# Kernel optimization log

Measured on AMD Instinct MI355X. Metric: run time of the kernel, lower is better.

Reference implementation:

```python
import jax, jax.numpy as jnp
import numpy as np

N_NODES = 50000
N_EDGES = 800000
N_FEAT = 128
HIDDEN = 128
N_GRAPHS = 256


def gcn_conv(x, W, b, src, dst, n_nodes):
    # PyG GCNConv, add_self_loops=False, edge_weight=1:
    # out_i = sum_{(j->i)} d_j^{-1/2} d_i^{-1/2} (x_j @ W) + b, deg over target idx
    h = x @ W                                    # [N, out]
    deg = jax.ops.segment_sum(jnp.ones((src.shape[0],), h.dtype), dst,
                              num_segments=n_nodes)          # [N]
    dis = jnp.where(deg > 0, jax.lax.rsqrt(jnp.maximum(deg, 1.0)), 0.0)
    norm = dis[src] * dis[dst]                   # [E]
    msg = h[src] * norm[:, None]                 # [E, out] gather + scale
    out = jax.ops.segment_sum(msg, dst, num_segments=n_nodes)  # scatter-add
    return out + b


def setup_inputs() -> dict:
    key = jax.random.key(0)
    ks = jax.random.split(key, 12)
    x = jax.random.normal(ks[0], (N_NODES, N_FEAT), jnp.float32)
    edge_index = jax.random.randint(ks[1], (2, N_EDGES), 0, N_NODES, jnp.int64)
    batch = jnp.sort(jax.random.randint(ks[2], (N_NODES,), 0, N_GRAPHS, jnp.int64))

    def glorot(k, shape):
        lim = float(np.sqrt(6.0 / (shape[0] + shape[1])))
        return jax.random.uniform(k, shape, jnp.float32, -lim, lim)

    W1 = glorot(ks[3], (N_FEAT, HIDDEN)); b1 = jnp.zeros((HIDDEN,), jnp.float32)
    W2 = glorot(ks[4], (HIDDEN, HIDDEN)); b2 = jnp.zeros((HIDDEN,), jnp.float32)
    Wf1 = glorot(ks[5], (HIDDEN, HIDDEN // 2)); bf1 = jnp.zeros((HIDDEN // 2,), jnp.float32)
    Wl = glorot(ks[6], (HIDDEN // 2, 2)); bl = jnp.zeros((2,), jnp.float32)
    return {"x": x, "edge_index": edge_index, "batch": batch,
            "W1": W1, "b1": b1, "W2": W2, "b2": b2,
            "Wf1": Wf1, "bf1": bf1, "Wl": Wl, "bl": bl}


def reference(x, edge_index, batch, W1, b1, W2, b2, Wf1, bf1, Wl, bl):
    src, dst = edge_index[0], edge_index[1]
    h = jax.nn.relu(gcn_conv(x, W1, b1, src, dst, N_NODES))
    h = jax.nn.relu(gcn_conv(h, W2, b2, src, dst, N_NODES))
    h = gcn_conv(h, W2, b2, src, dst, N_NODES)   # conv2 applied a second time (same weights)
    # global_mean_pool over graphs
    sums = jax.ops.segment_sum(h, batch, num_segments=N_GRAPHS)      # [G, H]
    cnts = jax.ops.segment_sum(jnp.ones((h.shape[0],), h.dtype), batch,
                               num_segments=N_GRAPHS)                # [G]
    g = sums / jnp.maximum(cnts, 1.0)[:, None]
    g = jax.nn.relu(g @ Wf1 + bf1)
    logits = g @ Wl + bl
    return jax.nn.softmax(logits, axis=1)
```

## Files before the change

### kernel.cpp

```cpp
#include <hip/hip_runtime.h>
#include <hip/hip_bf16.h>

#define N_NODES 50000
#define N_EDGES 800000
#define NF 128
#define NG 256
#define CAP 64
#define NSEG 256
#define SEGE (N_EDGES / NSEG)
#define NPAD 50048

typedef unsigned short ushort_t;
typedef unsigned char uchar_t;
typedef __attribute__((ext_vector_type(8))) short bf16x8;
typedef __attribute__((ext_vector_type(4))) float f32x4;

__device__ __forceinline__ float b2f(ushort_t u) {
    union { unsigned i; float f; } x; x.i = ((unsigned)u) << 16; return x.f;
}
__device__ __forceinline__ ushort_t f2b(float f) {
    union { float f; unsigned i; } x; x.f = f;
    unsigned r = (x.i + 0x7fffu + ((x.i >> 16) & 1u)) >> 16;
    return (ushort_t)r;
}

__global__ __launch_bounds__(512) void k_seg_count(
        const int* __restrict__ dst, uchar_t* __restrict__ segcnt,
        float* __restrict__ gsum) {
    __shared__ unsigned int cntw[NPAD / 4];
    int tid = threadIdx.x;
    int b = blockIdx.x;
    if (b < 16) {
        ((float4*)gsum)[b * 512 + tid] = make_float4(0.f, 0.f, 0.f, 0.f);
    }
    for (int i = tid; i < NPAD / 4; i += 512) cntw[i] = 0;
    __syncthreads();
    const int* d0 = dst + b * SEGE;
    for (int e = tid; e < SEGE; e += 512) {
        int d = d0[e];
        atomicAdd(&cntw[d >> 2], 1u << ((d & 3) * 8));
    }
    __syncthreads();
    unsigned int* outw = (unsigned int*)(segcnt + (size_t)b * NPAD);
    for (int i = tid; i < NPAD / 4; i += 512) outw[i] = cntw[i];
}

__global__ void k_seg_scan(const uchar_t* __restrict__ segcnt,
                           uchar_t* __restrict__ segbase,
                           int* __restrict__ deg, float* __restrict__ dis) {
    int node = blockIdx.x * 256 + threadIdx.x;
    if (node >= N_NODES) return;
    int run = 0;
#pragma unroll 8
    for (int s = 0; s < NSEG; ++s) {
        size_t idx = (size_t)s * NPAD + node;
        int c = segcnt[idx];
        segbase[idx] = (uchar_t)min(run, 255);
        run += c;
    }
    deg[node] = min(run, CAP);
    dis[node] = (run > 0) ? rsqrtf((float)run) : 0.f;
}

__global__ __launch_bounds__(512) void k_seg_fill(
        const int* __restrict__ src, const int* __restrict__ dst,
        const uchar_t* __restrict__ segbase, ushort_t* __restrict__ csr_pad) {
    __shared__ unsigned int cntw[NPAD / 4];
    int tid = threadIdx.x;
    int b = blockIdx.x;
    for (int i = tid; i < NPAD / 4; i += 512) cntw[i] = 0;
    __syncthreads();
    const int* d0 = dst + b * SEGE;
    const int* s0 = src + b * SEGE;
    const uchar_t* brow = segbase + (size_t)b * NPAD;
    for (int e = tid; e < SEGE; e += 512) {
        int d = d0[e];
        int sh = (d & 3) * 8;
        unsigned old = atomicAdd(&cntw[d >> 2], 1u << sh);
        int pos = (old >> sh) & 0xFF;
        int slot = brow[d] + pos;
        if (slot < CAP) csr_pad[(size_t)d * CAP + slot] = (ushort_t)s0[e];
    }
}

__global__ void k_prep_w2(const float* __restrict__ W1, const float* __restrict__ W2,
                          ushort_t* __restrict__ W1h, ushort_t* __restrict__ W1l,
                          ushort_t* __restrict__ W2h, ushort_t* __restrict__ W2l) {
    int t = blockIdx.x * blockDim.x + threadIdx.x;
    int which = t >> 14;
    int u = t & 16383;
    int k = u >> 7, c = u & 127;
    const float* W = which ? W2 : W1;
    ushort_t* Wh = which ? W2h : W1h;
    ushort_t* Wl = which ? W2l : W1l;
    float w = W[k * 128 + c];
    ushort_t hi = f2b(w);
    ushort_t lo = f2b(w - b2f(hi));
    Wh[c * 128 + k] = hi;
    Wl[c * 128 + k] = lo;
}

template <bool F32A>
__global__ __launch_bounds__(256) void k_gemm_mfma(
        const float* __restrict__ Xf, const ushort_t* __restrict__ Xb,
        const ushort_t* __restrict__ Wt_hi, const ushort_t* __restrict__ Wt_lo,
        const float* __restrict__ dis, ushort_t* __restrict__ Yb, int n) {
    __shared__ ushort_t Wlds[2][16384];
    int t = threadIdx.x;
    {
        const int4* gh = (const int4*)Wt_hi;
        const int4* gl = (const int4*)Wt_lo;
        int4* sh = (int4*)&Wlds[0][0];
        int4* sl = (int4*)&Wlds[1][0];
#pragma unroll
        for (int i = 0; i < 8; ++i) {
            int u = t + i * 256;
            int swz = u ^ ((u >> 4) & 7);
            sh[swz] = gh[u];
            sl[swz] = gl[u];
        }
    }
    __syncthreads();

    int wid = t >> 6;
    int l   = t & 63;
    int la  = l & 15;
    int kb  = l >> 4;
    int r0  = blockIdx.x * 64 + wid * 16;

    bf16x8 a[4];
    {
        int ra = min(r0 + la, n - 1);
        if (F32A) {
            const float* xrow = Xf + (size_t)ra * 128 + kb * 8;
#pragma unroll
            for (int kt = 0; kt < 4; ++kt) {
                float4 v0 = *(const float4*)(xrow + kt * 32);
                float4 v1 = *(const float4*)(xrow + kt * 32 + 4);
                bf16x8 av;
                av[0] = (short)f2b(v0.x); av[1] = (short)f2b(v0.y);
                av[2] = (short)f2b(v0.z); av[3] = (short)f2b(v0.w);
                av[4] = (short)f2b(v1.x); av[5] = (short)f2b(v1.y);
                av[6] = (short)f2b(v1.z); av[7] = (short)f2b(v1.w);
                a[kt] = av;
            }
        } else {
            const ushort_t* xrow = Xb + (size_t)ra * 128 + kb * 8;
#pragma unroll
            for (int kt = 0; kt < 4; ++kt)
                a[kt] = *(const bf16x8*)(xrow + kt * 32);
        }
    }

    f32x4 acc[8];
#pragma unroll
    for (int ct = 0; ct < 8; ++ct) acc[ct] = (f32x4){0.f, 0.f, 0.f, 0.f};

#pragma unroll
    for (int ct = 0; ct < 8; ++ct) {
        int c = ct * 16 + la;
        int ubase = c * 128 + kb * 8;
        int sw = (c & 7) << 3;
#pragma unroll
        for (int kt = 0; kt < 4; ++kt) {
            int u16 = (ubase + kt * 32) ^ sw;
            bf16x8 bh = *(const bf16x8*)&Wlds[0][u16];
            bf16x8 bl = *(const bf16x8*)&Wlds[1][u16];
            acc[ct] = __builtin_amdgcn_mfma_f32_16x16x32_bf16(a[kt], bh, acc[ct], 0, 0, 0);
            acc[ct] = __builtin_amdgcn_mfma_f32_16x16x32_bf16(a[kt], bl, acc[ct], 0, 0, 0);
        }
    }

    float dsc[4];
#pragma unroll
    for (int j = 0; j < 4; ++j)
        dsc[j] = dis[min(r0 + kb * 4 + j, n - 1)];

    __syncthreads();
    ushort_t* tile = ((ushort_t*)Wlds) + wid * 2048;
#pragma unroll
    for (int ct = 0; ct < 8; ++ct) {
        int cc = ct * 16 + la;
#pragma unroll
        for (int j = 0; j < 4; ++j)
            tile[(kb * 4 + j) * 128 + cc] = f2b(acc[ct][j] * dsc[j]);
    }
    __syncthreads();
    {
        const int4* t4 = (const int4*)tile;
        int4* dst4 = (int4*)(Yb + (size_t)r0 * 128);
#pragma unroll
        for (int i = 0; i < 4; ++i) {
            int u = l * 4 + i;
            int row = u >> 4;
            if (r0 + row < n) dst4[u] = t4[u];
        }
    }
}

template <bool RELU>
__global__ __launch_bounds__(256) void k_agg(
        const ushort_t* __restrict__ Hs, const int* __restrict__ deg,
        const ushort_t* __restrict__ csr_pad, const float* __restrict__ dis,
        const float* __restrict__ bias, ushort_t* __restrict__ out, int n) {
    int lane = threadIdx.x & 31;
    int sub  = threadIdx.x >> 5;
    int node = blockIdx.x * 8 + sub;
    if (node >= n) return;
    int dg = deg[node];
    const ushort_t* lst = csr_pad + (size_t)node * CAP;
    int c0 = lane * 4;

    float4 a0 = make_float4(0.f, 0.f, 0.f, 0.f);
    float4 a1 = make_float4(0.f, 0.f, 0.f, 0.f);
    float4 a2 = make_float4(0.f, 0.f, 0.f, 0.f);
    float4 a3 = make_float4(0.f, 0.f, 0.f, 0.f);
    float4 a4 = make_float4(0.f, 0.f, 0.f, 0.f);
    float4 a5 = make_float4(0.f, 0.f, 0.f, 0.f);
    float4 a6 = make_float4(0.f, 0.f, 0.f, 0.f);
    float4 a7 = make_float4(0.f, 0.f, 0.f, 0.f);
    int p = 0;
    for (; p + 7 < dg; p += 8) {
        int j0 = lst[p],     j1 = lst[p + 1], j2 = lst[p + 2], j3 = lst[p + 3];
        int j4 = lst[p + 4], j5 = lst[p + 5], j6 = lst[p + 6], j7 = lst[p + 7];
        ushort4 v0 = *(const ushort4*)&Hs[(size_t)j0 * 128 + c0];
        ushort4 v1 = *(const ushort4*)&Hs[(size_t)j1 * 128 + c0];
        ushort4 v2 = *(const ushort4*)&Hs[(size_t)j2 * 128 + c0];
        ushort4 v3 = *(const ushort4*)&Hs[(size_t)j3 * 128 + c0];
        ushort4 v4 = *(const ushort4*)&Hs[(size_t)j4 * 128 + c0];
        ushort4 v5 = *(const ushort4*)&Hs[(size_t)j5 * 128 + c0];
        ushort4 v6 = *(const ushort4*)&Hs[(size_t)j6 * 128 + c0];
        ushort4 v7 = *(const ushort4*)&Hs[(size_t)j7 * 128 + c0];
        a0.x += b2f(v0.x); a0.y += b2f(v0.y); a0.z += b2f(v0.z); a0.w += b2f(v0.w);
        a1.x += b2f(v1.x); a1.y += b2f(v1.y); a1.z += b2f(v1.z); a1.w += b2f(v1.w);
        a2.x += b2f(v2.x); a2.y += b2f(v2.y); a2.z += b2f(v2.z); a2.w += b2f(v2.w);
        a3.x += b2f(v3.x); a3.y += b2f(v3.y); a3.z += b2f(v3.z); a3.w += b2f(v3.w);
        a4.x += b2f(v4.x); a4.y += b2f(v4.y); a4.z += b2f(v4.z); a4.w += b2f(v4.w);
        a5.x += b2f(v5.x); a5.y += b2f(v5.y); a5.z += b2f(v5.z); a5.w += b2f(v5.w);
        a6.x += b2f(v6.x); a6.y += b2f(v6.y); a6.z += b2f(v6.z); a6.w += b2f(v6.w);
        a7.x += b2f(v7.x); a7.y += b2f(v7.y); a7.z += b2f(v7.z); a7.w += b2f(v7.w);
    }
    for (; p + 3 < dg; p += 4) {
        int j0 = lst[p], j1 = lst[p + 1], j2 = lst[p + 2], j3 = lst[p + 3];
        ushort4 v0 = *(const ushort4*)&Hs[(size_t)j0 * 128 + c0];
        ushort4 v1 = *(const ushort4*)&Hs[(size_t)j1 * 128 + c0];
        ushort4 v2 = *(const ushort4*)&Hs[(size_t)j2 * 128 + c0];
        ushort4 v3 = *(const ushort4*)&Hs[(size_t)j3 * 128 + c0];
        a0.x += b2f(v0.x); a0.y += b2f(v0.y); a0.z += b2f(v0.z); a0.w += b2f(v0.w);
        a1.x += b2f(v1.x); a1.y += b2f(v1.y); a1.z += b2f(v1.z); a1.w += b2f(v1.w);
        a2.x += b2f(v2.x); a2.y += b2f(v2.y); a2.z += b2f(v2.z); a2.w += b2f(v2.w);
        a3.x += b2f(v3.x); a3.y += b2f(v3.y); a3.z += b2f(v3.z); a3.w += b2f(v3.w);
    }
    for (; p < dg; ++p) {
        int j = lst[p];
        ushort4 v = *(const ushort4*)&Hs[(size_t)j * 128 + c0];
        a0.x += b2f(v.x); a0.y += b2f(v.y); a0.z += b2f(v.z); a0.w += b2f(v.w);
    }
    float dsc = dis[node];
    float4 b = *(const float4*)&bias[c0];
    float rx = (((a0.x + a1.x) + (a2.x + a3.x)) + ((a4.x + a5.x) + (a6.x + a7.x))) * dsc + b.x;
    float ry = (((a0.y + a1.y) + (a2.y + a3.y)) + ((a4.y + a5.y) + (a6.y + a7.y))) * dsc + b.y;
    float rz = (((a0.z + a1.z) + (a2.z + a3.z)) + ((a4.z + a5.z) + (a6.z + a7.z))) * dsc + b.z;
    float rw = (((a0.w + a1.w) + (a2.w + a3.w)) + ((a4.w + a5.w) + (a6.w + a7.w))) * dsc + b.w;
    if (RELU) {
        rx = fmaxf(rx, 0.f); ry = fmaxf(ry, 0.f);
        rz = fmaxf(rz, 0.f); rw = fmaxf(rw, 0.f);
    }
    ushort4 o;
    o.x = f2b(rx); o.y = f2b(ry); o.z = f2b(rz); o.w = f2b(rw);
    *(ushort4*)&out[(size_t)node * 128 + c0] = o;
}

#define POOL_CHUNK 128
__global__ __launch_bounds__(128) void k_pool_partial(
        const ushort_t* __restrict__ H, const int* __restrict__ batch,
        float* __restrict__ gsum, int n) {
    int f = threadIdx.x;
    int s = blockIdx.x * POOL_CHUNK;
    int e = min(s + POOL_CHUNK, n);
    if (s >= n) return;
    float acc = 0.f;
    int g = batch[s];
    for (int i = s; i < e; ++i) {
        int bg = batch[i];
        if (bg != g) {
            atomicAdd(&gsum[g * 128 + f], acc);
            acc = 0.f;
            g = bg;
        }
        acc += b2f(H[(size_t)i * 128 + f]);
    }
    atomicAdd(&gsum[g * 128 + f], acc);
}

__global__ void k_head(const float* __restrict__ gsum, const int* __restrict__ batch,
                       const float* __restrict__ Wf1, const float* __restrict__ bf1,
                       const float* __restrict__ Wl, const float* __restrict__ bl,
                       float* __restrict__ out, int n) {
    int g = blockIdx.x;
    int j = threadIdx.x;
    __shared__ float xs[128];
    __shared__ float hs[64];

    int lo = 0, hi = n;
    while (lo < hi) { int m = (lo + hi) >> 1; if (batch[m] < g) lo = m + 1; else hi = m; }
    int s0 = lo;
    hi = n;
    while (lo < hi) { int m = (lo + hi) >> 1; if (batch[m] <= g) lo = m + 1; else hi = m; }
    float inv_cnt = 1.f / fmaxf((float)(lo - s0), 1.f);

    xs[j]      = gsum[g * 128 + j] * inv_cnt;
    xs[j + 64] = gsum[g * 128 + 64 + j] * inv_cnt;
    __syncthreads();
    float acc = bf1[j];
#pragma unroll 4
    for (int k = 0; k < 128; k++) acc += xs[k] * Wf1[k * 64 + j];
    hs[j] = fmaxf(acc, 0.f);
    __syncthreads();
    if (j == 0) {
        float l0 = bl[0], l1 = bl[1];
        for (int k = 0; k < 64; k++) { l0 += hs[k] * Wl[k * 2 + 0]; l1 += hs[k] * Wl[k * 2 + 1]; }
        float m  = fmaxf(l0, l1);
        float e0 = expf(l0 - m), e1 = expf(l1 - m);
        float inv = 1.f / (e0 + e1);
        out[g * 2 + 0] = e0 * inv;
        out[g * 2 + 1] = e1 * inv;
    }
}

extern "C" void kernel_launch(void* const* d_in, const int* in_sizes, int n_in,
                              void* d_out, int out_size, void* d_ws, size_t ws_size,
                              hipStream_t stream) {
    const float* x    = (const float*)d_in[0];
    const int*   eidx = (const int*)d_in[1];
    const int*   batch= (const int*)d_in[2];
    const float* W1   = (const float*)d_in[3];
    const float* b1   = (const float*)d_in[4];
    const float* W2   = (const float*)d_in[5];
    const float* b2   = (const float*)d_in[6];
    const float* Wf1  = (const float*)d_in[7];
    const float* bf1  = (const float*)d_in[8];
    const float* Wl   = (const float*)d_in[9];
    const float* bl   = (const float*)d_in[10];
    float* out = (float*)d_out;

    const int* src = eidx;
    const int* dst = eidx + N_EDGES;

    char* w = (char*)d_ws;
    auto alloc = [&](size_t bytes) -> void* {
        void* p = (void*)w;
        w += (bytes + 255) & ~(size_t)255;
        return p;
    };
    ushort_t* Yb     = (ushort_t*)alloc((size_t)N_NODES * NF * 2);
    ushort_t* Hb     = (ushort_t*)alloc((size_t)N_NODES * NF * 2);
    ushort_t* W1h    = (ushort_t*)alloc((size_t)NF * NF * 2);
    ushort_t* W1l    = (ushort_t*)alloc((size_t)NF * NF * 2);
    ushort_t* W2h    = (ushort_t*)alloc((size_t)NF * NF * 2);
    ushort_t* W2l    = (ushort_t*)alloc((size_t)NF * NF * 2);
    float*    dis    = (float*)alloc((size_t)N_NODES * 4);
    int*      deg    = (int*)  alloc((size_t)N_NODES * 4);
    ushort_t* csr_pad= (ushort_t*)alloc((size_t)N_NODES * CAP * 2);
    uchar_t*  segcnt = (uchar_t*)alloc((size_t)NSEG * NPAD);
    uchar_t*  segbase= (uchar_t*)alloc((size_t)NSEG * NPAD);
    float*    gsum   = (float*)alloc((size_t)NG * NF * 4);

    k_seg_count<<<NSEG, 512, 0, stream>>>(dst, segcnt, gsum);
    k_seg_scan<<<(N_NODES + 255) / 256, 256, 0, stream>>>(segcnt, segbase, deg, dis);
    k_seg_fill<<<NSEG, 512, 0, stream>>>(src, dst, segbase, csr_pad);

    k_prep_w2<<<128, 256, 0, stream>>>(W1, W2, W1h, W1l, W2h, W2l);

    int gb = (N_NODES + 63) / 64;
    int ab = (N_NODES + 7) / 8;
    k_gemm_mfma<true><<<gb, 256, 0, stream>>>(x, nullptr, W1h, W1l, dis, Yb, N_NODES);
    k_agg<true><<<ab, 256, 0, stream>>>(Yb, deg, csr_pad, dis, b1, Hb, N_NODES);
    k_gemm_mfma<false><<<gb, 256, 0, stream>>>(nullptr, Hb, W2h, W2l, dis, Yb, N_NODES);
    k_agg<true><<<ab, 256, 0, stream>>>(Yb, deg, csr_pad, dis, b2, Hb, N_NODES);
    k_gemm_mfma<false><<<gb, 256, 0, stream>>>(nullptr, Hb, W2h, W2l, dis, Yb, N_NODES);
    k_agg<false><<<ab, 256, 0, stream>>>(Yb, deg, csr_pad, dis, b2, Hb, N_NODES);

    k_pool_partial<<<(N_NODES + POOL_CHUNK - 1) / POOL_CHUNK, 128, 0, stream>>>(Hb, batch, gsum, N_NODES);
    k_head<<<NG, 64, 0, stream>>>(gsum, batch, Wf1, bf1, Wl, bl, out, N_NODES);
}
```

Before: 234.6 us.

## Fuse aggregation with next-layer GEMM and fold weight prep into CSR fill

```diff
diff --git a/kernel.cpp b/kernel.cpp
--- a/kernel.cpp
+++ b/kernel.cpp
@@ -9,6 +9,7 @@
 #define NSEG 256
 #define SEGE (N_EDGES / NSEG)
 #define NPAD 50048
+#define NPREPB 16
 
 typedef unsigned short ushort_t;
 typedef unsigned char uchar_t;
@@ -64,10 +65,32 @@
 
 __global__ __launch_bounds__(512) void k_seg_fill(
         const int* __restrict__ src, const int* __restrict__ dst,
-        const uchar_t* __restrict__ segbase, ushort_t* __restrict__ csr_pad) {
+        const uchar_t* __restrict__ segbase, ushort_t* __restrict__ csr_pad,
+        const float* __restrict__ W1, const float* __restrict__ W2,
+        ushort_t* __restrict__ W1h, ushort_t* __restrict__ W1l,
+        ushort_t* __restrict__ W2h, ushort_t* __restrict__ W2l) {
     __shared__ unsigned int cntw[NPAD / 4];
     int tid = threadIdx.x;
     int b = blockIdx.x;
+    if (b >= NSEG) {
+        int base = (b - NSEG) * 2048 + tid * 4;
+#pragma unroll
+        for (int i = 0; i < 4; ++i) {
+            int id = base + i;
+            int which = id >> 14;
+            int u = id & 16383;
+            int k = u >> 7, c = u & 127;
+            const float* W = which ? W2 : W1;
+            ushort_t* Wh = which ? W2h : W1h;
+            ushort_t* Wl = which ? W2l : W1l;
+            float w = W[k * 128 + c];
+            ushort_t hi = f2b(w);
+            ushort_t lo = f2b(w - b2f(hi));
+            Wh[c * 128 + k] = hi;
+            Wl[c * 128 + k] = lo;
+        }
+        return;
+    }
     for (int i = tid; i < NPAD / 4; i += 512) cntw[i] = 0;
     __syncthreads();
     const int* d0 = dst + b * SEGE;
@@ -83,26 +106,8 @@
     }
 }
 
-__global__ void k_prep_w2(const float* __restrict__ W1, const float* __restrict__ W2,
-                          ushort_t* __restrict__ W1h, ushort_t* __restrict__ W1l,
-                          ushort_t* __restrict__ W2h, ushort_t* __restrict__ W2l) {
-    int t = blockIdx.x * blockDim.x + threadIdx.x;
-    int which = t >> 14;
-    int u = t & 16383;
-    int k = u >> 7, c = u & 127;
-    const float* W = which ? W2 : W1;
-    ushort_t* Wh = which ? W2h : W1h;
-    ushort_t* Wl = which ? W2l : W1l;
-    float w = W[k * 128 + c];
-    ushort_t hi = f2b(w);
-    ushort_t lo = f2b(w - b2f(hi));
-    Wh[c * 128 + k] = hi;
-    Wl[c * 128 + k] = lo;
-}
-
-template <bool F32A>
 __global__ __launch_bounds__(256) void k_gemm_mfma(
-        const float* __restrict__ Xf, const ushort_t* __restrict__ Xb,
+        const float* __restrict__ Xf,
         const ushort_t* __restrict__ Wt_hi, const ushort_t* __restrict__ Wt_lo,
         const float* __restrict__ dis, ushort_t* __restrict__ Yb, int n) {
     __shared__ ushort_t Wlds[2][16384];
@@ -131,24 +136,17 @@
     bf16x8 a[4];
     {
         int ra = min(r0 + la, n - 1);
-        if (F32A) {
-            const float* xrow = Xf + (size_t)ra * 128 + kb * 8;
-#pragma unroll
-            for (int kt = 0; kt < 4; ++kt) {
-                float4 v0 = *(const float4*)(xrow + kt * 32);
-                float4 v1 = *(const float4*)(xrow + kt * 32 + 4);
-                bf16x8 av;
-                av[0] = (short)f2b(v0.x); av[1] = (short)f2b(v0.y);
-                av[2] = (short)f2b(v0.z); av[3] = (short)f2b(v0.w);
-                av[4] = (short)f2b(v1.x); av[5] = (short)f2b(v1.y);
-                av[6] = (short)f2b(v1.z); av[7] = (short)f2b(v1.w);
-                a[kt] = av;
-            }
-        } else {
-            const ushort_t* xrow = Xb + (size_t)ra * 128 + kb * 8;
-#pragma unroll
-            for (int kt = 0; kt < 4; ++kt)
-                a[kt] = *(const bf16x8*)(xrow + kt * 32);
+        const float* xrow = Xf + (size_t)ra * 128 + kb * 8;
+#pragma unroll
+        for (int kt = 0; kt < 4; ++kt) {
+            float4 v0 = *(const float4*)(xrow + kt * 32);
+            float4 v1 = *(const float4*)(xrow + kt * 32 + 4);
+            bf16x8 av;
+            av[0] = (short)f2b(v0.x); av[1] = (short)f2b(v0.y);
+            av[2] = (short)f2b(v0.z); av[3] = (short)f2b(v0.w);
+            av[4] = (short)f2b(v1.x); av[5] = (short)f2b(v1.y);
+            av[6] = (short)f2b(v1.z); av[7] = (short)f2b(v1.w);
+            a[kt] = av;
         }
     }
 
@@ -198,8 +196,143 @@
     }
 }
 
-template <bool RELU>
-__global__ __launch_bounds__(256) void k_agg(
+__global__ __launch_bounds__(256) void k_agg_gemm(
+        const ushort_t* __restrict__ Yin, const int* __restrict__ deg,
+        const ushort_t* __restrict__ csr_pad, const float* __restrict__ dis,
+        const float* __restrict__ bias,
+        const ushort_t* __restrict__ Wt_hi, const ushort_t* __restrict__ Wt_lo,
+        ushort_t* __restrict__ Yout, int n) {
+    __shared__ ushort_t tile[64][132];
+    int t = threadIdx.x;
+    int lane = t & 31, sub = t >> 5;
+    int r0 = blockIdx.x * 64;
+    int c0 = lane * 4;
+
+    for (int it = 0; it < 8; ++it) {
+        int local = it * 8 + sub;
+        int node = r0 + local;
+        ushort4 o = make_ushort4(0, 0, 0, 0);
+        if (node < n) {
+            int dg = deg[node];
+            const ushort_t* lst = csr_pad + (size_t)node * CAP;
+            float4 a0 = make_float4(0.f, 0.f, 0.f, 0.f);
+            float4 a1 = make_float4(0.f, 0.f, 0.f, 0.f);
+            float4 a2 = make_float4(0.f, 0.f, 0.f, 0.f);
+            float4 a3 = make_float4(0.f, 0.f, 0.f, 0.f);
+            float4 a4 = make_float4(0.f, 0.f, 0.f, 0.f);
+            float4 a5 = make_float4(0.f, 0.f, 0.f, 0.f);
+            float4 a6 = make_float4(0.f, 0.f, 0.f, 0.f);
+            float4 a7 = make_float4(0.f, 0.f, 0.f, 0.f);
+            int p = 0;
+            for (; p + 7 < dg; p += 8) {
+                int j0 = lst[p],     j1 = lst[p + 1], j2 = lst[p + 2], j3 = lst[p + 3];
+                int j4 = lst[p + 4], j5 = lst[p + 5], j6 = lst[p + 6], j7 = lst[p + 7];
+                ushort4 v0 = *(const ushort4*)&Yin[(size_t)j0 * 128 + c0];
+                ushort4 v1 = *(const ushort4*)&Yin[(size_t)j1 * 128 + c0];
+                ushort4 v2 = *(const ushort4*)&Yin[(size_t)j2 * 128 + c0];
+                ushort4 v3 = *(const ushort4*)&Yin[(size_t)j3 * 128 + c0];
+                ushort4 v4 = *(const ushort4*)&Yin[(size_t)j4 * 128 + c0];
+                ushort4 v5 = *(const ushort4*)&Yin[(size_t)j5 * 128 + c0];
+                ushort4 v6 = *(const ushort4*)&Yin[(size_t)j6 * 128 + c0];
+                ushort4 v7 = *(const ushort4*)&Yin[(size_t)j7 * 128 + c0];
+                a0.x += b2f(v0.x); a0.y += b2f(v0.y); a0.z += b2f(v0.z); a0.w += b2f(v0.w);
+                a1.x += b2f(v1.x); a1.y += b2f(v1.y); a1.z += b2f(v1.z); a1.w += b2f(v1.w);
+                a2.x += b2f(v2.x); a2.y += b2f(v2.y); a2.z += b2f(v2.z); a2.w += b2f(v2.w);
+                a3.x += b2f(v3.x); a3.y += b2f(v3.y); a3.z += b2f(v3.z); a3.w += b2f(v3.w);
+                a4.x += b2f(v4.x); a4.y += b2f(v4.y); a4.z += b2f(v4.z); a4.w += b2f(v4.w);
+                a5.x += b2f(v5.x); a5.y += b2f(v5.y); a5.z += b2f(v5.z); a5.w += b2f(v5.w);
+                a6.x += b2f(v6.x); a6.y += b2f(v6.y); a6.z += b2f(v6.z); a6.w += b2f(v6.w);
+                a7.x += b2f(v7.x); a7.y += b2f(v7.y); a7.z += b2f(v7.z); a7.w += b2f(v7.w);
+            }
+            for (; p + 3 < dg; p += 4) {
+                int j0 = lst[p], j1 = lst[p + 1], j2 = lst[p + 2], j3 = lst[p + 3];
+                ushort4 v0 = *(const ushort4*)&Yin[(size_t)j0 * 128 + c0];
+                ushort4 v1 = *(const ushort4*)&Yin[(size_t)j1 * 128 + c0];
+                ushort4 v2 = *(const ushort4*)&Yin[(size_t)j2 * 128 + c0];
+                ushort4 v3 = *(const ushort4*)&Yin[(size_t)j3 * 128 + c0];
+                a0.x += b2f(v0.x); a0.y += b2f(v0.y); a0.z += b2f(v0.z); a0.w += b2f(v0.w);
+                a1.x += b2f(v1.x); a1.y += b2f(v1.y); a1.z += b2f(v1.z); a1.w += b2f(v1.w);
+                a2.x += b2f(v2.x); a2.y += b2f(v2.y); a2.z += b2f(v2.z); a2.w += b2f(v2.w);
+                a3.x += b2f(v3.x); a3.y += b2f(v3.y); a3.z += b2f(v3.z); a3.w += b2f(v3.w);
+            }
+            for (; p < dg; ++p) {
+                int j = lst[p];
+                ushort4 v = *(const ushort4*)&Yin[(size_t)j * 128 + c0];
+                a0.x += b2f(v.x); a0.y += b2f(v.y); a0.z += b2f(v.z); a0.w += b2f(v.w);
+            }
+            float dsc = dis[node];
+            float4 b = *(const float4*)&bias[c0];
+            float rx = (((a0.x + a1.x) + (a2.x + a3.x)) + ((a4.x + a5.x) + (a6.x + a7.x))) * dsc + b.x;
+            float ry = (((a0.y + a1.y) + (a2.y + a3.y)) + ((a4.y + a5.y) + (a6.y + a7.y))) * dsc + b.y;
+            float rz = (((a0.z + a1.z) + (a2.z + a3.z)) + ((a4.z + a5.z) + (a6.z + a7.z))) * dsc + b.z;
+            float rw = (((a0.w + a1.w) + (a2.w + a3.w)) + ((a4.w + a5.w) + (a6.w + a7.w))) * dsc + b.w;
+            rx = fmaxf(rx, 0.f); ry = fmaxf(ry, 0.f);
+            rz = fmaxf(rz, 0.f); rw = fmaxf(rw, 0.f);
+            o.x = f2b(rx); o.y = f2b(ry); o.z = f2b(rz); o.w = f2b(rw);
+        }
+        *(ushort4*)&tile[local][c0] = o;
+    }
+    __syncthreads();
+
+    int wid = t >> 6;
+    int l   = t & 63;
+    int la  = l & 15;
+    int kb  = l >> 4;
+
+    bf16x8 a[4];
+    {
+        const ushort_t* arow = &tile[wid * 16 + la][kb * 8];
+#pragma unroll
+        for (int kt = 0; kt < 4; ++kt)
+            a[kt] = *(const bf16x8*)(arow + kt * 32);
+    }
+
+    f32x4 acc[8];
+#pragma unroll
+    for (int ct = 0; ct < 8; ++ct) acc[ct] = (f32x4){0.f, 0.f, 0.f, 0.f};
+
+#pragma unroll
+    for (int ct = 0; ct < 8; ++ct) {
+        int c = ct * 16 + la;
+        const ushort_t* bh_p = Wt_hi + c * 128 + kb * 8;
+        const ushort_t* bl_p = Wt_lo + c * 128 + kb * 8;
+#pragma unroll
+        for (int kt = 0; kt < 4; ++kt) {
+            bf16x8 bh = *(const bf16x8*)(bh_p + kt * 32);
+            bf16x8 bl = *(const bf16x8*)(bl_p + kt * 32);
+            acc[ct] = __builtin_amdgcn_mfma_f32_16x16x32_bf16(a[kt], bh, acc[ct], 0, 0, 0);
+            acc[ct] = __builtin_amdgcn_mfma_f32_16x16x32_bf16(a[kt], bl, acc[ct], 0, 0, 0);
+        }
+    }
+
+    float dsc2[4];
+#pragma unroll
+    for (int j = 0; j < 4; ++j)
+        dsc2[j] = dis[min(r0 + wid * 16 + kb * 4 + j, n - 1)];
+
+    __syncthreads();
+    ushort_t* otile = ((ushort_t*)tile) + wid * 2048;
+#pragma unroll
+    for (int ct = 0; ct < 8; ++ct) {
+        int cc = ct * 16 + la;
+#pragma unroll
+        for (int j = 0; j < 4; ++j)
+            otile[(kb * 4 + j) * 128 + cc] = f2b(acc[ct][j] * dsc2[j]);
+    }
+    __syncthreads();
+    {
+        const int4* t4 = (const int4*)otile;
+        int4* dst4 = (int4*)(Yout + (size_t)(r0 + wid * 16) * 128);
+#pragma unroll
+        for (int i = 0; i < 4; ++i) {
+            int u = l * 4 + i;
+            int row = u >> 4;
+            if (r0 + wid * 16 + row < n) dst4[u] = t4[u];
+        }
+    }
+}
+
+__global__ __launch_bounds__(256) void k_agg_final(
         const ushort_t* __restrict__ Hs, const int* __restrict__ deg,
         const ushort_t* __restrict__ csr_pad, const float* __restrict__ dis,
         const float* __restrict__ bias, ushort_t* __restrict__ out, int n) {
@@ -262,10 +395,6 @@
     float ry = (((a0.y + a1.y) + (a2.y + a3.y)) + ((a4.y + a5.y) + (a6.y + a7.y))) * dsc + b.y;
     float rz = (((a0.z + a1.z) + (a2.z + a3.z)) + ((a4.z + a5.z) + (a6.z + a7.z))) * dsc + b.z;
     float rw = (((a0.w + a1.w) + (a2.w + a3.w)) + ((a4.w + a5.w) + (a6.w + a7.w))) * dsc + b.w;
-    if (RELU) {
-        rx = fmaxf(rx, 0.f); ry = fmaxf(ry, 0.f);
-        rz = fmaxf(rz, 0.f); rw = fmaxf(rw, 0.f);
-    }
     ushort4 o;
     o.x = f2b(rx); o.y = f2b(ry); o.z = f2b(rz); o.w = f2b(rw);
     *(ushort4*)&out[(size_t)node * 128 + c0] = o;
@@ -368,18 +497,14 @@
 
     k_seg_count<<<NSEG, 512, 0, stream>>>(dst, segcnt, gsum);
     k_seg_scan<<<(N_NODES + 255) / 256, 256, 0, stream>>>(segcnt, segbase, deg, dis);
-    k_seg_fill<<<NSEG, 512, 0, stream>>>(src, dst, segbase, csr_pad);
-
-    k_prep_w2<<<128, 256, 0, stream>>>(W1, W2, W1h, W1l, W2h, W2l);
+    k_seg_fill<<<NSEG + NPREPB, 512, 0, stream>>>(src, dst, segbase, csr_pad,
+                                                  W1, W2, W1h, W1l, W2h, W2l);
 
     int gb = (N_NODES + 63) / 64;
-    int ab = (N_NODES + 7) / 8;
-    k_gemm_mfma<true><<<gb, 256, 0, stream>>>(x, nullptr, W1h, W1l, dis, Yb, N_NODES);
-    k_agg<true><<<ab, 256, 0, stream>>>(Yb, deg, csr_pad, dis, b1, Hb, N_NODES);
-    k_gemm_mfma<false><<<gb, 256, 0, stream>>>(nullptr, Hb, W2h, W2l, dis, Yb, N_NODES);
-    k_agg<true><<<ab, 256, 0, stream>>>(Yb, deg, csr_pad, dis, b2, Hb, N_NODES);
-    k_gemm_mfma<false><<<gb, 256, 0, stream>>>(nullptr, Hb, W2h, W2l, dis, Yb, N_NODES);
-    k_agg<false><<<ab, 256, 0, stream>>>(Yb, deg, csr_pad, dis, b2, Hb, N_NODES);
+    k_gemm_mfma<<<gb, 256, 0, stream>>>(x, W1h, W1l, dis, Yb, N_NODES);
+    k_agg_gemm<<<gb, 256, 0, stream>>>(Yb, deg, csr_pad, dis, b1, W2h, W2l, Hb, N_NODES);
+    k_agg_gemm<<<gb, 256, 0, stream>>>(Hb, deg, csr_pad, dis, b2, W2h, W2l, Yb, N_NODES);
+    k_agg_final<<<(N_NODES + 7) / 8, 256, 0, stream>>>(Yb, deg, csr_pad, dis, b2, Hb, N_NODES);
 
     k_pool_partial<<<(N_NODES + POOL_CHUNK - 1) / POOL_CHUNK, 128, 0, stream>>>(Hb, batch, gsum, N_NODES);
     k_head<<<NG, 64, 0, stream>>>(gsum, batch, Wf1, bf1, Wl, bl, out, N_NODES);
```

Measured after the change: 276.9 us. +18.0%, slower.
